# Optimization experiments

Hardware: AMD Instinct MI355X
Metric: run time of the kernel (lower is better)

The kernel has to match this reference:

```python
import jax, jax.numpy as jnp
import numpy as np

N_NODES = 100000
N_EDGES = 1600000
DIM = 64
NUM_HEADS = 4
HEAD_DIM = DIM // NUM_HEADS
QK_SCALE = HEAD_DIM ** -0.5
EPS = 1e-16  # matches torch_geometric softmax denominator eps


def setup_inputs() -> dict:
    key = jax.random.key(0)
    k1, k2, k3 = jax.random.split(key, 3)
    x = jax.random.normal(k1, (N_NODES, DIM), dtype=jnp.float32)
    W_qkv = jax.random.normal(k2, (DIM, 3 * DIM), dtype=jnp.float32) * (DIM ** -0.5)
    b_qkv = jnp.zeros((3 * DIM,), dtype=jnp.float32)
    edge_index = jax.random.randint(k3, (2, N_EDGES), 0, N_NODES, dtype=jnp.int64)
    return {"x": x, "W_qkv": W_qkv, "b_qkv": b_qkv, "edge_index": edge_index}


def reference(x, W_qkv, b_qkv, edge_index):
    N = x.shape[0]
    E = edge_index.shape[1]
    # qkv projection: (N, 3, H, d)
    qkv = (x @ W_qkv + b_qkv).reshape(N, 3, NUM_HEADS, HEAD_DIM)
    s = edge_index[0]  # query (source) node per edge
    t = edge_index[1]  # key/value (target) node per edge
    q = qkv[s, 0] * QK_SCALE  # (E, H, d)
    k = qkv[t, 1]             # (E, H, d)
    v = qkv[t, 2]             # (E, H, d)
    compat = jnp.einsum('ehd,ehd->eh', q, k)  # (E, H)
    # segment softmax keyed by source node (numerically stable)
    m = jax.ops.segment_max(compat, s, num_segments=N)          # (N, H)
    ex = jnp.exp(compat - m[s])                                  # (E, H)
    den = jax.ops.segment_sum(ex, s, num_segments=N)             # (N, H)
    attn = ex / (den[s] + EPS)                                   # (E, H)
    # weighted values, flatten heads, scatter-sum back to source nodes
    msg = (v * attn[..., None]).reshape(E, DIM)                  # (E, dim)
    out = jax.ops.segment_sum(msg, s, num_segments=N)            # (N, dim)
    return out
```

## Files before the change

### kernel.cpp

```cpp
#include <hip/hip_runtime.h>

constexpr int N_NODES = 100000;
constexpr int N_EDGES = 1600000;
constexpr int DIM = 64;
constexpr float QK_SCALE = 0.25f;
constexpr float EPS = 1e-16f;

constexpr int NBK = (N_NODES + 255) / 256;
constexpr int BCAP = 8192;
constexpr int SC_CHUNK = 8192;
constexpr int SC_THREADS = 512;
constexpr int SC_BLOCKS = (N_EDGES + SC_CHUNK - 1) / SC_CHUNK;

typedef __attribute__((ext_vector_type(8))) short short8;
typedef __attribute__((ext_vector_type(4))) float f32x4;

__device__ __forceinline__ unsigned short f32_to_bf16_rne(float f) {
    unsigned int u = __float_as_uint(f);
    u += 0x7fffu + ((u >> 16) & 1u);
    return (unsigned short)(u >> 16);
}

__device__ __forceinline__ int orig_col(int jp) {
    if (jp < 64) return jp;
    const int p = jp - 64;
    const int chunk = p >> 3, w = p & 7;
    return (w < 4) ? (64 + chunk * 4 + w) : (128 + chunk * 4 + (w - 4));
}

__global__ __launch_bounds__(192) void prep_w(const float* __restrict__ W,
                                              const float* __restrict__ b,
                                              unsigned short* __restrict__ Wbt,
                                              float* __restrict__ bb,
                                              int* __restrict__ bcnt) {
    const int jp = threadIdx.x;
    const int oc = orig_col(jp);
    const float sc = (jp < 64) ? QK_SCALE : 1.f;
    for (int k = 0; k < DIM; ++k)
        Wbt[jp * DIM + k] = f32_to_bf16_rne(W[k * 192 + oc] * sc);
    bb[jp] = b[oc] * sc;
    for (int i = jp; i < NBK; i += 192) bcnt[i] = 0;
}

__global__ __launch_bounds__(256) void qkv_mfma(const float* __restrict__ x,
                                                const unsigned short* __restrict__ Wbt,
                                                const float* __restrict__ bb,
                                                float* __restrict__ q_arr,
                                                unsigned short* __restrict__ kv) {
    const int lane = threadIdx.x & 63;
    const int wid = threadIdx.x >> 6;
    const int n0 = blockIdx.x * 64 + wid * 16;
    if (n0 >= N_NODES) return;
    const int row = lane & 15;
    const int kg = lane >> 4;

    const int nidx = min(n0 + row, N_NODES - 1);
    const float* xr = x + (size_t)nidx * DIM + kg * 8;
    short8 a0, a1;
    {
        const float4 u0 = *(const float4*)(xr);
        const float4 u1 = *(const float4*)(xr + 4);
        const float4 u2 = *(const float4*)(xr + 32);
        const float4 u3 = *(const float4*)(xr + 36);
        a0[0] = (short)f32_to_bf16_rne(u0.x); a0[1] = (short)f32_to_bf16_rne(u0.y);
        a0[2] = (short)f32_to_bf16_rne(u0.z); a0[3] = (short)f32_to_bf16_rne(u0.w);
        a0[4] = (short)f32_to_bf16_rne(u1.x); a0[5] = (short)f32_to_bf16_rne(u1.y);
        a0[6] = (short)f32_to_bf16_rne(u1.z); a0[7] = (short)f32_to_bf16_rne(u1.w);
        a1[0] = (short)f32_to_bf16_rne(u2.x); a1[1] = (short)f32_to_bf16_rne(u2.y);
        a1[2] = (short)f32_to_bf16_rne(u2.z); a1[3] = (short)f32_to_bf16_rne(u2.w);
        a1[4] = (short)f32_to_bf16_rne(u3.x); a1[5] = (short)f32_to_bf16_rne(u3.y);
        a1[6] = (short)f32_to_bf16_rne(u3.z); a1[7] = (short)f32_to_bf16_rne(u3.w);
    }

    #pragma unroll
    for (int ct = 0; ct < 12; ++ct) {
        const int c0 = ct * 16;
        const float bias = bb[c0 + row];
        f32x4 acc = {bias, bias, bias, bias};
        const short8 b0 = *(const short8*)(Wbt + (c0 + row) * DIM + kg * 8);
        const short8 b1 = *(const short8*)(Wbt + (c0 + row) * DIM + kg * 8 + 32);
        acc = __builtin_amdgcn_mfma_f32_16x16x32_bf16(a0, b0, acc, 0, 0, 0);
        acc = __builtin_amdgcn_mfma_f32_16x16x32_bf16(a1, b1, acc, 0, 0, 0);

        const int colg = c0 + row;
        #pragma unroll
        for (int r = 0; r < 4; ++r) {
            const int node = n0 + kg * 4 + r;
            if (node < N_NODES) {
                if (c0 < 64) q_arr[(size_t)node * 64 + colg] = acc[r];
                else kv[(size_t)node * 128 + (colg - 64)] = f32_to_bf16_rne(acc[r]);
            }
        }
    }
}

__global__ __launch_bounds__(SC_THREADS) void bucket_scatter(const int* __restrict__ ei,
                                                             int* __restrict__ bcnt,
                                                             unsigned int* __restrict__ bbuf) {
    __shared__ int h[NBK];
    __shared__ int lofs[NBK];
    __shared__ int gbase[NBK];
    __shared__ int wsum[SC_THREADS / 64];
    __shared__ unsigned int stage[SC_CHUNK];

    const int tid = threadIdx.x;
    const int lane = tid & 63;
    const int wid = tid >> 6;
    const int e0 = blockIdx.x * SC_CHUNK;
    const int n = min(SC_CHUNK, N_EDGES - e0);

    for (int i = tid; i < NBK; i += SC_THREADS) h[i] = 0;
    __syncthreads();

    for (int i = tid; i < n; i += SC_THREADS)
        atomicAdd(&h[ei[e0 + i] >> 8], 1);
    __syncthreads();

    const int v = (tid < NBK) ? h[tid] : 0;
    int inc = v;
    #pragma unroll
    for (int d = 1; d < 64; d <<= 1) {
        int u = __shfl_up(inc, d);
        if (lane >= d) inc += u;
    }
    if (lane == 63) wsum[wid] = inc;
    __syncthreads();
    int woff = 0;
    for (int w = 0; w < wid; ++w) woff += wsum[w];
    if (tid < NBK) lofs[tid] = woff + inc - v;
    if (tid < NBK) gbase[tid] = (v > 0) ? atomicAdd(&bcnt[tid], v) : 0;
    __syncthreads();

    for (int i = tid; i < NBK; i += SC_THREADS) h[i] = 0;
    __syncthreads();

    for (int i = tid; i < n; i += SC_THREADS) {
        const int s = ei[e0 + i];
        const int t = ei[N_EDGES + e0 + i];
        const int bk = s >> 8;
        const int c = atomicAdd(&h[bk], 1);
        stage[lofs[bk] + c] = (unsigned int)t | ((unsigned int)(s & 255) << 17);
    }
    __syncthreads();

    for (int bk = wid; bk < NBK; bk += SC_THREADS / 64) {
        const int cnt = h[bk];
        const int lo = lofs[bk];
        unsigned int* dst = bbuf + (size_t)bk * BCAP + gbase[bk];
        for (int i = lane; i < cnt; i += 64) dst[i] = stage[lo + i];
    }
}

__global__ __launch_bounds__(256) void csr_build(const int* __restrict__ bcnt,
                                                 const unsigned int* __restrict__ bbuf,
                                                 int* __restrict__ deg,
                                                 int* __restrict__ off,
                                                 int* __restrict__ sorted_t) {
    __shared__ int h[256];
    __shared__ int lofs[256];
    __shared__ int wsum[4];
    __shared__ int sBase;

    const int tid = threadIdx.x;
    const int lane = tid & 63;
    const int wid = tid >> 6;
    const int bk = blockIdx.x;
    const int n = bcnt[bk];

    int pre = 0;
    for (int i = tid; i < bk; i += 256) pre += bcnt[i];
    #pragma unroll
    for (int d = 1; d < 64; d <<= 1) pre += __shfl_xor(pre, d);
    if (lane == 0) wsum[wid] = pre;
    h[tid] = 0;
    __syncthreads();
    if (tid == 0) sBase = wsum[0] + wsum[1] + wsum[2] + wsum[3];
    __syncthreads();

    const unsigned int* p = bbuf + (size_t)bk * BCAP;
    for (int i = tid; i < n; i += 256)
        atomicAdd(&h[p[i] >> 17], 1);
    __syncthreads();

    const int v = h[tid];
    int inc = v;
    #pragma unroll
    for (int d = 1; d < 64; d <<= 1) {
        int u = __shfl_up(inc, d);
        if (lane >= d) inc += u;
    }
    if (lane == 63) wsum[wid] = inc;
    __syncthreads();
    int woff = 0;
    for (int w = 0; w < wid; ++w) woff += wsum[w];
    const int exc = woff + inc - v;
    lofs[tid] = exc;
    const int node = bk * 256 + tid;
    if (node < N_NODES) { deg[node] = v; off[node] = sBase + exc; }
    __syncthreads();

    h[tid] = 0;
    __syncthreads();
    int* dstbase = sorted_t + sBase;
    for (int i = tid; i < n; i += 256) {
        const unsigned int e = p[i];
        const int s8 = e >> 17;
        const int c = atomicAdd(&h[s8], 1);
        dstbase[lofs[s8] + c] = (int)(e & 0x1FFFFu);
    }
}

__global__ __launch_bounds__(256) void node_pass(const float* __restrict__ q_arr,
                                                 const unsigned short* __restrict__ kv,
                                                 const int* __restrict__ off,
                                                 const int* __restrict__ deg,
                                                 const int* __restrict__ sorted_t,
                                                 float* __restrict__ out) {
    const int node = blockIdx.x * 4 + (threadIdx.x >> 6);
    const int lane = threadIdx.x & 63;
    if (node >= N_NODES) return;
    const int eg = lane >> 4;
    const int q16 = lane & 15;

    const int o = off[node];
    const int d = deg[node];

    const float4 qv = *(const float4*)(q_arr + (size_t)node * 64 + q16 * 4);
    const float NEG_INF = -__builtin_inff();
    float m = NEG_INF;
    float l = 0.f;
    float4 acc = make_float4(0.f, 0.f, 0.f, 0.f);

    for (int base = 0; base < d; base += 64) {
        const int nb = min(64, d - base);
        int tb = (base + lane < d) ? sorted_t[o + base + lane] : 0;
        for (int j8 = 0; j8 < nb; j8 += 8) {
            const int ia = j8 + eg;
            const int ib = j8 + 4 + eg;
            const int ta = __shfl(tb, ia);
            const int tc = __shfl(tb, ib);
            const uint4 A = *(const uint4*)(kv + (size_t)ta * 128 + q16 * 8);
            const uint4 B = *(const uint4*)(kv + (size_t)tc * 128 + q16 * 8);
            float pa = qv.x * __uint_as_float(A.x << 16)
                     + qv.y * __uint_as_float(A.x & 0xffff0000u)
                     + qv.z * __uint_as_float(A.y << 16)
                     + qv.w * __uint_as_float(A.y & 0xffff0000u);
            float pb = qv.x * __uint_as_float(B.x << 16)
                     + qv.y * __uint_as_float(B.x & 0xffff0000u)
                     + qv.z * __uint_as_float(B.y << 16)
                     + qv.w * __uint_as_float(B.y & 0xffff0000u);
            pa += __shfl_xor(pa, 1);  pb += __shfl_xor(pb, 1);
            pa += __shfl_xor(pa, 2);  pb += __shfl_xor(pb, 2);
            pa = (ia < nb) ? pa : NEG_INF;
            pb = (ib < nb) ? pb : NEG_INF;
            float pm = fmaxf(pa, pb);
            pm = fmaxf(pm, __shfl_xor(pm, 16));
            pm = fmaxf(pm, __shfl_xor(pm, 32));
            if (__any(pm > m)) {
                const float nm = fmaxf(m, pm);
                const float sc = __expf(m - nm);
                l *= sc;
                acc.x *= sc; acc.y *= sc; acc.z *= sc; acc.w *= sc;
                m = nm;
            }
            const float ea = __expf(pa - m);
            const float eb = __expf(pb - m);
            l += ea + eb;
            acc.x = fmaf(ea, __uint_as_float(A.z << 16),
                    fmaf(eb, __uint_as_float(B.z << 16),         acc.x));
            acc.y = fmaf(ea, __uint_as_float(A.z & 0xffff0000u),
                    fmaf(eb, __uint_as_float(B.z & 0xffff0000u), acc.y));
            acc.z = fmaf(ea, __uint_as_float(A.w << 16),
                    fmaf(eb, __uint_as_float(B.w << 16),         acc.z));
            acc.w = fmaf(ea, __uint_as_float(A.w & 0xffff0000u),
                    fmaf(eb, __uint_as_float(B.w & 0xffff0000u), acc.w));
        }
    }
    l += __shfl_xor(l, 16);  l += __shfl_xor(l, 32);
    acc.x += __shfl_xor(acc.x, 16);  acc.x += __shfl_xor(acc.x, 32);
    acc.y += __shfl_xor(acc.y, 16);  acc.y += __shfl_xor(acc.y, 32);
    acc.z += __shfl_xor(acc.z, 16);  acc.z += __shfl_xor(acc.z, 32);
    acc.w += __shfl_xor(acc.w, 16);  acc.w += __shfl_xor(acc.w, 32);

    if (eg == 0) {
        const float inv = 1.f / (l + EPS);
        float4 r = make_float4(acc.x * inv, acc.y * inv, acc.z * inv, acc.w * inv);
        *(float4*)(out + (size_t)node * DIM + q16 * 4) = r;
    }
}

extern "C" void kernel_launch(void* const* d_in, const int* in_sizes, int n_in,
                              void* d_out, int out_size, void* d_ws, size_t ws_size,
                              hipStream_t stream) {
    const float* x = (const float*)d_in[0];
    const float* W = (const float*)d_in[1];
    const float* b = (const float*)d_in[2];
    const int*   ei = (const int*)d_in[3];
    float* out = (float*)d_out;

    float* q_arr = (float*)d_ws;
    unsigned short* kv = (unsigned short*)(q_arr + (size_t)N_NODES * 64);
    unsigned int* bbuf = (unsigned int*)(kv + (size_t)N_NODES * 128);
    int* sorted_t = (int*)(bbuf + (size_t)NBK * BCAP);
    int* deg      = sorted_t + N_EDGES;
    int* off      = deg + N_NODES;
    int* bcnt     = off + N_NODES;
    unsigned short* Wbt = (unsigned short*)(bcnt + NBK);
    float* bb     = (float*)(Wbt + 192 * DIM);

    prep_w<<<1, 192, 0, stream>>>(W, b, Wbt, bb, bcnt);
    qkv_mfma<<<(N_NODES + 63) / 64, 256, 0, stream>>>(x, Wbt, bb, q_arr, kv);
    bucket_scatter<<<SC_BLOCKS, SC_THREADS, 0, stream>>>(ei, bcnt, bbuf);
    csr_build<<<NBK, 256, 0, stream>>>(bcnt, bbuf, deg, off, sorted_t);
    node_pass<<<(N_NODES + 3) / 4, 256, 0, stream>>>(q_arr, kv, off, deg, sorted_t, out);
}
```

Baseline: 139.5 us.

## Store Q in bf16 in unified QKV buffer, fold log2e, unroll node pass by four

```diff
diff --git a/kernel.cpp b/kernel.cpp
--- a/kernel.cpp
+++ b/kernel.cpp
@@ -4,6 +4,7 @@
 constexpr int N_EDGES = 1600000;
 constexpr int DIM = 64;
 constexpr float QK_SCALE = 0.25f;
+constexpr float LOG2E = 1.4426950408889634f;
 constexpr float EPS = 1e-16f;
 
 constexpr int NBK = (N_NODES + 255) / 256;
@@ -19,6 +20,16 @@
     unsigned int u = __float_as_uint(f);
     u += 0x7fffu + ((u >> 16) & 1u);
     return (unsigned short)(u >> 16);
+}
+__device__ __forceinline__ float bf_lo(unsigned int u) { return __uint_as_float(u << 16); }
+__device__ __forceinline__ float bf_hi(unsigned int u) { return __uint_as_float(u & 0xffff0000u); }
+
+__device__ __forceinline__ float qsum4(float p) {
+    int a = __builtin_amdgcn_update_dpp(0, __float_as_int(p), 0xB1, 0xF, 0xF, true);
+    p += __int_as_float(a);
+    int c = __builtin_amdgcn_update_dpp(0, __float_as_int(p), 0x4E, 0xF, 0xF, true);
+    p += __int_as_float(c);
+    return p;
 }
 
 __device__ __forceinline__ int orig_col(int jp) {
@@ -34,19 +45,20 @@
                                               float* __restrict__ bb,
                                               int* __restrict__ bcnt) {
     const int jp = threadIdx.x;
+    const int k = blockIdx.x;
     const int oc = orig_col(jp);
-    const float sc = (jp < 64) ? QK_SCALE : 1.f;
-    for (int k = 0; k < DIM; ++k)
-        Wbt[jp * DIM + k] = f32_to_bf16_rne(W[k * 192 + oc] * sc);
-    bb[jp] = b[oc] * sc;
-    for (int i = jp; i < NBK; i += 192) bcnt[i] = 0;
+    const float sc = (jp < 64) ? QK_SCALE * LOG2E : 1.f;
+    Wbt[jp * DIM + k] = f32_to_bf16_rne(W[k * 192 + oc] * sc);
+    if (k == 0) {
+        bb[jp] = b[oc] * sc;
+        for (int i = jp; i < NBK; i += 192) bcnt[i] = 0;
+    }
 }
 
 __global__ __launch_bounds__(256) void qkv_mfma(const float* __restrict__ x,
                                                 const unsigned short* __restrict__ Wbt,
                                                 const float* __restrict__ bb,
-                                                float* __restrict__ q_arr,
-                                                unsigned short* __restrict__ kv) {
+                                                unsigned short* __restrict__ qkv_t) {
     const int lane = threadIdx.x & 63;
     const int wid = threadIdx.x >> 6;
     const int n0 = blockIdx.x * 64 + wid * 16;
@@ -86,10 +98,8 @@
         #pragma unroll
         for (int r = 0; r < 4; ++r) {
             const int node = n0 + kg * 4 + r;
-            if (node < N_NODES) {
-                if (c0 < 64) q_arr[(size_t)node * 64 + colg] = acc[r];
-                else kv[(size_t)node * 128 + (colg - 64)] = f32_to_bf16_rne(acc[r]);
-            }
+            if (node < N_NODES)
+                qkv_t[(size_t)node * 192 + colg] = f32_to_bf16_rne(acc[r]);
         }
     }
 }
@@ -210,8 +220,7 @@
     }
 }
 
-__global__ __launch_bounds__(256) void node_pass(const float* __restrict__ q_arr,
-                                                 const unsigned short* __restrict__ kv,
+__global__ __launch_bounds__(256) void node_pass(const unsigned short* __restrict__ qkv,
                                                  const int* __restrict__ off,
                                                  const int* __restrict__ deg,
                                                  const int* __restrict__ sorted_t,
@@ -225,7 +234,10 @@
     const int o = off[node];
     const int d = deg[node];
 
-    const float4 qv = *(const float4*)(q_arr + (size_t)node * 64 + q16 * 4);
+    const uint2 qu = *(const uint2*)(qkv + (size_t)node * 192 + q16 * 4);
+    const float qx = bf_lo(qu.x), qy = bf_hi(qu.x);
+    const float qz = bf_lo(qu.y), qw = bf_hi(qu.y);
+
     const float NEG_INF = -__builtin_inff();
     float m = NEG_INF;
     float l = 0.f;
@@ -234,46 +246,48 @@
     for (int base = 0; base < d; base += 64) {
         const int nb = min(64, d - base);
         int tb = (base + lane < d) ? sorted_t[o + base + lane] : 0;
-        for (int j8 = 0; j8 < nb; j8 += 8) {
-            const int ia = j8 + eg;
-            const int ib = j8 + 4 + eg;
-            const int ta = __shfl(tb, ia);
-            const int tc = __shfl(tb, ib);
-            const uint4 A = *(const uint4*)(kv + (size_t)ta * 128 + q16 * 8);
-            const uint4 B = *(const uint4*)(kv + (size_t)tc * 128 + q16 * 8);
-            float pa = qv.x * __uint_as_float(A.x << 16)
-                     + qv.y * __uint_as_float(A.x & 0xffff0000u)
-                     + qv.z * __uint_as_float(A.y << 16)
-                     + qv.w * __uint_as_float(A.y & 0xffff0000u);
-            float pb = qv.x * __uint_as_float(B.x << 16)
-                     + qv.y * __uint_as_float(B.x & 0xffff0000u)
-                     + qv.z * __uint_as_float(B.y << 16)
-                     + qv.w * __uint_as_float(B.y & 0xffff0000u);
-            pa += __shfl_xor(pa, 1);  pb += __shfl_xor(pb, 1);
-            pa += __shfl_xor(pa, 2);  pb += __shfl_xor(pb, 2);
-            pa = (ia < nb) ? pa : NEG_INF;
-            pb = (ib < nb) ? pb : NEG_INF;
-            float pm = fmaxf(pa, pb);
+        for (int j16 = 0; j16 < nb; j16 += 16) {
+            const int i0 = j16 + eg;
+            const int t0 = __shfl(tb, i0);
+            const int t1 = __shfl(tb, i0 + 4);
+            const int t2 = __shfl(tb, i0 + 8);
+            const int t3 = __shfl(tb, i0 + 12);
+            const uint4 A0 = *(const uint4*)(qkv + (size_t)t0 * 192 + 64 + q16 * 8);
+            const uint4 A1 = *(const uint4*)(qkv + (size_t)t1 * 192 + 64 + q16 * 8);
+            const uint4 A2 = *(const uint4*)(qkv + (size_t)t2 * 192 + 64 + q16 * 8);
+            const uint4 A3 = *(const uint4*)(qkv + (size_t)t3 * 192 + 64 + q16 * 8);
+            float p0 = qx * bf_lo(A0.x) + qy * bf_hi(A0.x) + qz * bf_lo(A0.y) + qw * bf_hi(A0.y);
+            float p1 = qx * bf_lo(A1.x) + qy * bf_hi(A1.x) + qz * bf_lo(A1.y) + qw * bf_hi(A1.y);
+            float p2 = qx * bf_lo(A2.x) + qy * bf_hi(A2.x) + qz * bf_lo(A2.y) + qw * bf_hi(A2.y);
+            float p3 = qx * bf_lo(A3.x) + qy * bf_hi(A3.x) + qz * bf_lo(A3.y) + qw * bf_hi(A3.y);
+            p0 = qsum4(p0); p1 = qsum4(p1); p2 = qsum4(p2); p3 = qsum4(p3);
+            p0 = (i0      < nb) ? p0 : NEG_INF;
+            p1 = (i0 + 4  < nb) ? p1 : NEG_INF;
+            p2 = (i0 + 8  < nb) ? p2 : NEG_INF;
+            p3 = (i0 + 12 < nb) ? p3 : NEG_INF;
+            float pm = fmaxf(fmaxf(p0, p1), fmaxf(p2, p3));
             pm = fmaxf(pm, __shfl_xor(pm, 16));
             pm = fmaxf(pm, __shfl_xor(pm, 32));
             if (__any(pm > m)) {
                 const float nm = fmaxf(m, pm);
-                const float sc = __expf(m - nm);
+                const float sc = exp2f(m - nm);
                 l *= sc;
                 acc.x *= sc; acc.y *= sc; acc.z *= sc; acc.w *= sc;
                 m = nm;
             }
-            const float ea = __expf(pa - m);
-            const float eb = __expf(pb - m);
-            l += ea + eb;
-            acc.x = fmaf(ea, __uint_as_float(A.z << 16),
-                    fmaf(eb, __uint_as_float(B.z << 16),         acc.x));
-            acc.y = fmaf(ea, __uint_as_float(A.z & 0xffff0000u),
-                    fmaf(eb, __uint_as_float(B.z & 0xffff0000u), acc.y));
-            acc.z = fmaf(ea, __uint_as_float(A.w << 16),
-                    fmaf(eb, __uint_as_float(B.w << 16),         acc.z));
-            acc.w = fmaf(ea, __uint_as_float(A.w & 0xffff0000u),
-                    fmaf(eb, __uint_as_float(B.w & 0xffff0000u), acc.w));
+            const float e0 = exp2f(p0 - m);
+            const float e1 = exp2f(p1 - m);
+            const float e2 = exp2f(p2 - m);
+            const float e3 = exp2f(p3 - m);
+            l += (e0 + e1) + (e2 + e3);
+            acc.x = fmaf(e0, bf_lo(A0.z), fmaf(e1, bf_lo(A1.z),
+                    fmaf(e2, bf_lo(A2.z), fmaf(e3, bf_lo(A3.z), acc.x))));
+            acc.y = fmaf(e0, bf_hi(A0.z), fmaf(e1, bf_hi(A1.z),
+                    fmaf(e2, bf_hi(A2.z), fmaf(e3, bf_hi(A3.z), acc.y))));
+            acc.z = fmaf(e0, bf_lo(A0.w), fmaf(e1, bf_lo(A1.w),
+                    fmaf(e2, bf_lo(A2.w), fmaf(e3, bf_lo(A3.w), acc.z))));
+            acc.w = fmaf(e0, bf_hi(A0.w), fmaf(e1, bf_hi(A1.w),
+                    fmaf(e2, bf_hi(A2.w), fmaf(e3, bf_hi(A3.w), acc.w))));
         }
     }
     l += __shfl_xor(l, 16);  l += __shfl_xor(l, 32);
@@ -298,9 +312,8 @@
     const int*   ei = (const int*)d_in[3];
     float* out = (float*)d_out;
 
-    float* q_arr = (float*)d_ws;
-    unsigned short* kv = (unsigned short*)(q_arr + (size_t)N_NODES * 64);
-    unsigned int* bbuf = (unsigned int*)(kv + (size_t)N_NODES * 128);
+    unsigned short* qkv_t = (unsigned short*)d_ws;
+    unsigned int* bbuf = (unsigned int*)(qkv_t + (size_t)N_NODES * 192);
     int* sorted_t = (int*)(bbuf + (size_t)NBK * BCAP);
     int* deg      = sorted_t + N_EDGES;
     int* off      = deg + N_NODES;
@@ -308,9 +321,9 @@
     unsigned short* Wbt = (unsigned short*)(bcnt + NBK);
     float* bb     = (float*)(Wbt + 192 * DIM);
 
-    prep_w<<<1, 192, 0, stream>>>(W, b, Wbt, bb, bcnt);
-    qkv_mfma<<<(N_NODES + 63) / 64, 256, 0, stream>>>(x, Wbt, bb, q_arr, kv);
+    prep_w<<<64, 192, 0, stream>>>(W, b, Wbt, bb, bcnt);
+    qkv_mfma<<<(N_NODES + 63) / 64, 256, 0, stream>>>(x, Wbt, bb, qkv_t);
     bucket_scatter<<<SC_BLOCKS, SC_THREADS, 0, stream>>>(ei, bcnt, bbuf);
     csr_build<<<NBK, 256, 0, stream>>>(bcnt, bbuf, deg, off, sorted_t);
-    node_pass<<<(N_NODES + 3) / 4, 256, 0, stream>>>(q_arr, kv, off, deg, sorted_t, out);
-}
+    node_pass<<<(N_NODES + 3) / 4, 256, 0, stream>>>(qkv_t, off, deg, sorted_t, out);
+}
```

Measured after the change: 135.1 us. -3.1%, faster.
